# Performance work log

Hardware: AMD Instinct MI355X
Metric: run time of the kernel (lower is better)

Reference implementation:

```python
import jax, jax.numpy as jnp
import numpy as np

IN_DIM, OUT_DIM, N_BLOCKS, BLK_DIM = 256, 4, 2, 128
S, B = 1024, 128


def _u(key, shape, fan):
    lim = 1.0 / np.sqrt(fan)
    return jax.random.uniform(key, shape, jnp.float32, -lim, lim)


def _gru_params(key, i, h):
    k = jax.random.split(key, 4)
    return (_u(k[0], (3 * h, i), h), _u(k[1], (3 * h, h), h),
            _u(k[2], (3 * h,), h), _u(k[3], (3 * h,), h))


def gru_layer(x, wih, whh, bih, bhh):
    # x: (S, B, I) -> outputs (S, B, H); PyTorch GRU gate math, h0 = 0
    Bt = x.shape[1]
    H = whh.shape[1]
    xg = jnp.einsum('sbi,gi->sbg', x, wih) + bih  # (S, B, 3H) precomputed input gates

    def step(h, xg_t):
        hg = h @ whh.T + bhh
        xr, xz, xn = jnp.split(xg_t, 3, axis=-1)
        hr, hz, hn = jnp.split(hg, 3, axis=-1)
        r = jax.nn.sigmoid(xr + hr)
        z = jax.nn.sigmoid(xz + hz)
        n = jnp.tanh(xn + r * hn)
        h_new = (1.0 - z) * n + z * h
        return h_new, h_new

    h0 = jnp.zeros((Bt, H), x.dtype)
    _, ys = jax.lax.scan(step, h0, xg)
    return ys


def layernorm(x, g, b, eps=1e-5):
    m = jnp.mean(x, axis=-1, keepdims=True)
    v = jnp.mean(jnp.square(x - m), axis=-1, keepdims=True)
    return (x - m) * jax.lax.rsqrt(v + eps) * g + b


def setup_inputs() -> dict:
    key = jax.random.key(0)
    ks = jax.random.split(key, 16)
    d = {'x': jax.random.normal(ks[0], (S, B, IN_DIM), jnp.float32)}
    for nm, (i, h), kk in [('gru0', (IN_DIM, 2 * IN_DIM), ks[1]),
                           ('gru1', (IN_DIM // 2, IN_DIM), ks[2]),
                           ('gru2', (IN_DIM // 4, IN_DIM // 2), ks[3])]:
        wih, whh, bih, bhh = _gru_params(kk, i, h)
        d[nm + '_wih'], d[nm + '_whh'], d[nm + '_bih'], d[nm + '_bhh'] = wih, whh, bih, bhh
    d['d0_w'] = _u(ks[4], (BLK_DIM, 3 * 2 * IN_DIM), 3 * 2 * IN_DIM)
    d['d0_b'] = _u(ks[5], (BLK_DIM,), 3 * 2 * IN_DIM)
    for bi in range(N_BLOCKS):
        kb = jax.random.split(ks[6 + bi], 2)
        d[f'blk{bi}_ln_g'] = jnp.ones((BLK_DIM,), jnp.float32)
        d[f'blk{bi}_ln_b'] = jnp.zeros((BLK_DIM,), jnp.float32)
        wih, whh, bih, bhh = _gru_params(kb[0], BLK_DIM, BLK_DIM)
        d[f'blk{bi}_wih'], d[f'blk{bi}_whh'] = wih, whh
        d[f'blk{bi}_bih'], d[f'blk{bi}_bhh'] = bih, bhh
    d['df_w'] = _u(ks[10], (OUT_DIM, BLK_DIM), BLK_DIM)
    d['df_b'] = _u(ks[11], (OUT_DIM,), BLK_DIM)
    return d


def reference(x,
              gru0_wih, gru0_whh, gru0_bih, gru0_bhh,
              gru1_wih, gru1_whh, gru1_bih, gru1_bhh,
              gru2_wih, gru2_whh, gru2_bih, gru2_bhh,
              d0_w, d0_b,
              blk0_ln_g, blk0_ln_b, blk0_wih, blk0_whh, blk0_bih, blk0_bhh,
              blk1_ln_g, blk1_ln_b, blk1_wih, blk1_whh, blk1_bih, blk1_bhh,
              df_w, df_b):
    # branch 0: full-resolution features
    x0 = gru_layer(x, gru0_wih, gru0_whh, gru0_bih, gru0_bhh)            # (S,B,512)
    # branch 1: nearest-downsample features x0.5, GRU, nearest-upsample x2
    x1 = gru_layer(x[..., ::2], gru1_wih, gru1_whh, gru1_bih, gru1_bhh)  # (S,B,256)
    x1 = jnp.repeat(x1, 2, axis=-1)                                       # (S,B,512)
    # branch 2: nearest-downsample features x0.25, GRU, nearest-upsample x4
    x2 = gru_layer(x[..., ::4], gru2_wih, gru2_whh, gru2_bih, gru2_bhh)  # (S,B,128)
    x2 = jnp.repeat(x2, 4, axis=-1)                                       # (S,B,512)
    h = jnp.concatenate((x0, x1, x2), axis=-1)                            # (S,B,1536)
    h = jax.nn.relu(h @ d0_w.T + d0_b)                                    # (S,B,128)
    for (lg, lb, wih, whh, bih, bhh) in (
            (blk0_ln_g, blk0_ln_b, blk0_wih, blk0_whh, blk0_bih, blk0_bhh),
            (blk1_ln_g, blk1_ln_b, blk1_wih, blk1_whh, blk1_bih, blk1_bhh)):
        h = h + gru_layer(layernorm(h, lg, lb), wih, whh, bih, bhh)       # LN->GRU->residual
    return h @ df_w.T + df_b                                              # (S,B,4)
```

## Files before the change

kernel.cpp:

```cpp
#include <hip/hip_runtime.h>

typedef unsigned int u32;
typedef unsigned short u16;
typedef __attribute__((ext_vector_type(8))) short short8;
typedef __attribute__((ext_vector_type(4))) float f4;

#define MFMA16 __builtin_amdgcn_mfma_f32_16x16x32_bf16
#define ALOAD(p)    __hip_atomic_load((p), __ATOMIC_RELAXED, __HIP_MEMORY_SCOPE_AGENT)
#define ASTORE(p,v) __hip_atomic_store((p), (v), __ATOMIC_RELAXED, __HIP_MEMORY_SCOPE_AGENT)

#define OFF_XB    0LL
#define OFF_XD2   67108864LL
#define OFF_XD4   100663296LL
#define OFF_HCAT  117440512LL
#define OFF_LNB   352321536LL
#define OFF_H0R   385875968LL
#define OFF_Y0R   419430400LL
#define OFF_HB0   419561472LL
#define OFF_HB1   419823616LL
#define OFF_FLG   419954688LL
#define OFF_D0WF  420020224LL

__device__ __forceinline__ u16 f2bf(float f) {
  u32 u = __float_as_uint(f);
  return (u16)((u + 0x7fffu + ((u >> 16) & 1u)) >> 16);
}
__device__ __forceinline__ float bf2f(u32 b) { return __uint_as_float(b << 16); }
__device__ __forceinline__ float sigm(float x) { return __builtin_amdgcn_rcpf(1.f + __expf(-x)); }
__device__ __forceinline__ float tanh_(float x) { return 1.f - 2.f * __builtin_amdgcn_rcpf(1.f + __expf(2.f * x)); }

__device__ __forceinline__ short8 cvt8(const float* p) {
  short8 r;
#pragma unroll
  for (int j = 0; j < 8; ++j) r[j] = (short)f2bf(p[j]);
  return r;
}

template<int KH, int KX, int BT, int CSPAN, int WAVES, int GROUP_WGS, int PUB>
__device__ __forceinline__ void gru_scan(
    const float* __restrict__ wih, const float* __restrict__ whh,
    const float* __restrict__ bih, const float* __restrict__ bhh,
    const u16* __restrict__ xsrc,
    u16* __restrict__ outp, const int outPitch, const int outColBase,
    const int group, const int slab,
    u32* __restrict__ hbA, u32* __restrict__ hbB, u32* __restrict__ flags,
    char* sm)
{
  constexpr int H = KH;
  constexpr int KT = (KH + KX) / 32;
  constexpr int KH32 = KH / 32;
  constexpr int PITCH = (KH + KX) * 2 + 32;
  constexpr int CT_N = CSPAN / 16;
  constexpr int NTILES = (BT / 16) * CT_N;
  constexpr int MAXP = (NTILES + WAVES - 1) / WAVES;
  constexpr int NT = WAVES * 64;
  constexpr int NX = (BT * KX / 2) / NT;
  constexpr int NH = (BT * KH / 2) / NT;
  constexpr bool GH = (GROUP_WGS > 0);

  const int tid = threadIdx.x;
  const int l = tid & 63;
  const int wv = __builtin_amdgcn_readfirstlane(tid >> 6);
  const int lr = l & 15;
  const int lh = l >> 4;
  const long srow0 = group * BT;

  short8 Br[MAXP][KT], Bz[MAXP][KT], Bn[MAXP][KT];
  float bb0[MAXP], bb1[MAXP], bb2[MAXP], bb3[MAXP];
  float hk[MAXP][4];
#pragma unroll
  for (int p = 0; p < MAXP; ++p) {
    const int tp = wv + WAVES * p;
    const int tpc = (tp < NTILES) ? tp : 0;
    const int ct = tpc % CT_N;
    const int gcol = slab * CSPAN + ct * 16 + lr;
#pragma unroll
    for (int t = 0; t < KT; ++t) {
      const int k = t * 32 + lh * 8;
      if (t < KH32) {
        Br[p][t] = cvt8(whh + (long)(0 * H + gcol) * KH + k);
        Bz[p][t] = cvt8(whh + (long)(1 * H + gcol) * KH + k);
        Bn[p][t] = cvt8(whh + (long)(2 * H + gcol) * KH + k);
      } else {
        const int kx = k - KH;
        Br[p][t] = cvt8(wih + (long)(0 * H + gcol) * KX + kx);
        Bz[p][t] = cvt8(wih + (long)(1 * H + gcol) * KX + kx);
        Bn[p][t] = cvt8(wih + (long)(2 * H + gcol) * KX + kx);
      }
    }
    bb0[p] = bih[0 * H + gcol] + bhh[0 * H + gcol];
    bb1[p] = bih[1 * H + gcol] + bhh[1 * H + gcol];
    bb2[p] = bih[2 * H + gcol];
    bb3[p] = bhh[2 * H + gcol];
    hk[p][0] = hk[p][1] = hk[p][2] = hk[p][3] = 0.f;
  }

  if constexpr (!GH) {
#pragma unroll
    for (int i = 0; i < (BT * KH / 2 + NT - 1) / NT; ++i) {
      const int idx = tid + NT * i;
      if (idx < BT * KH / 2) {
        const int r = idx / (KH / 2), d = idx % (KH / 2);
        *(u32*)(sm + r * PITCH + ((d * 4) ^ ((r & 7) << 4))) = 0u;
      }
    }
  }

  u32 xr[NX];
#pragma unroll
  for (int i = 0; i < NX; ++i) {
    const int idx = tid + NT * i;
    const int r = idx / (KX / 2), d = idx % (KX / 2);
    xr[i] = *(const u32*)(xsrc + (srow0 + r) * KX + d * 2);
  }

  for (int s = 0; s < 1024; ++s) {
    if constexpr (GH) {
      if (wv == 0) {
        const u32 tgt = (u32)s;
        for (;;) {
          const u32 f = (l < GROUP_WGS) ? ALOAD(flags + l * 16) : tgt;
          if (__all(f >= tgt)) break;
        }
      }
      __builtin_amdgcn_s_barrier();
    }
#pragma unroll
    for (int i = 0; i < NX; ++i) {
      const int idx = tid + NT * i;
      const int r = idx / (KX / 2), d = idx % (KX / 2);
      *(u32*)(sm + r * PITCH + ((KH * 2 + d * 4) ^ ((r & 7) << 4))) = xr[i];
    }
    if constexpr (GH) {
      const u32* hb = (s & 1) ? hbB : hbA;
#pragma unroll
      for (int i = 0; i < NH; ++i) {
        const int idx = tid + NT * i;
        const int r = idx / (KH / 2), d = idx % (KH / 2);
        const u32 v = ALOAD(hb + r * (KH / 2) + d);
        *(u32*)(sm + r * PITCH + ((d * 4) ^ ((r & 7) << 4))) = v;
      }
    }
    if constexpr (!(GH || PUB)) {
      if (s + 1 < 1024) {
#pragma unroll
        for (int i = 0; i < NX; ++i) {
          const int idx = tid + NT * i;
          const int r = idx / (KX / 2), d = idx % (KX / 2);
          xr[i] = *(const u32*)(xsrc + ((s + 1) * 128L + srow0 + r) * KX + d * 2);
        }
      }
    }
    __syncthreads();

    u32 hnew[MAXP][4];
#pragma unroll
    for (int p = 0; p < MAXP; ++p) {
      const int tp = wv + WAVES * p;
      if (tp < NTILES) {
        const int mt = tp / CT_N;
        f4 ar = {0.f, 0.f, 0.f, 0.f}; f4 az = ar, anh = ar, anx = ar;
#pragma unroll
        for (int t = 0; t < KT; ++t) {
          const int row = mt * 16 + lr;
          const short8 a = *(const short8*)(sm + row * PITCH +
                              ((t * 64 + lh * 16) ^ ((row & 7) << 4)));
          ar = MFMA16(a, Br[p][t], ar, 0, 0, 0);
          az = MFMA16(a, Bz[p][t], az, 0, 0, 0);
          if (t < KH32) anh = MFMA16(a, Bn[p][t], anh, 0, 0, 0);
          else          anx = MFMA16(a, Bn[p][t], anx, 0, 0, 0);
        }
#pragma unroll
        for (int q = 0; q < 4; ++q) {
          const float rg = sigm(ar[q] + bb0[p]);
          const float zg = sigm(az[q] + bb1[p]);
          const float ng = tanh_(anx[q] + bb2[p] + rg * (anh[q] + bb3[p]));
          const float h = (1.f - zg) * ng + zg * hk[p][q];
          hk[p][q] = h;
          hnew[p][q] = f2bf(h);
        }
      }
    }
    if constexpr (!GH) __syncthreads();

    u32 pkv[MAXP][4];
#pragma unroll
    for (int p = 0; p < MAXP; ++p) {
      const int tp = wv + WAVES * p;
      if (tp < NTILES) {
        const int mt = tp / CT_N, ct = tp % CT_N;
        const int c = ct * 16 + lr;
#pragma unroll
        for (int q = 0; q < 4; ++q) {
          const u32 nb = (u32)__shfl_xor((int)hnew[p][q], 1);
          pkv[p][q] = (hnew[p][q] & 0xffffu) | (nb << 16);
          if ((l & 1) == 0) {
            const int b = mt * 16 + lh * 4 + q;
            if constexpr (GH) {
              u32* hbn = ((s + 1) & 1) ? hbB : hbA;
              ASTORE(hbn + b * (KH / 2) + (slab * CSPAN + c) / 2, pkv[p][q]);
            } else {
              *(u32*)(sm + b * PITCH + ((c * 2) ^ ((b & 7) << 4))) = pkv[p][q];
            }
          }
        }
      }
    }
    __builtin_amdgcn_sched_barrier(0);
#pragma unroll
    for (int p = 0; p < MAXP; ++p) {
      const int tp = wv + WAVES * p;
      if (tp < NTILES) {
        const int mt = tp / CT_N, ct = tp % CT_N;
        const int c = ct * 16 + lr;
#pragma unroll
        for (int q = 0; q < 4; ++q) {
          if ((l & 1) == 0) {
            const int b = mt * 16 + lh * 4 + q;
            u32* oa = (u32*)(outp + (s * 128L + srow0 + b) * outPitch + outColBase + c);
            if constexpr (GH || PUB) ASTORE(oa, pkv[p][q]); else *oa = pkv[p][q];
          }
        }
      }
    }
    if constexpr (GH) {
      __builtin_amdgcn_sched_barrier(0);
      if (s + 1 < 1024) {
#pragma unroll
        for (int i = 0; i < NX; ++i) {
          const int idx = tid + NT * i;
          const int r = idx / (KX / 2), d = idx % (KX / 2);
          xr[i] = ALOAD((const u32*)(xsrc + ((s + 1) * 128L + srow0 + r) * KX + d * 2));
        }
        __builtin_amdgcn_sched_barrier(0);
        asm volatile("s_waitcnt vmcnt(%0)" :: "i"(MAXP * 4 + NX) : "memory");
      } else {
        asm volatile("s_waitcnt vmcnt(0)" ::: "memory");
      }
      __builtin_amdgcn_s_barrier();
      if (tid == 0) ASTORE(flags + slab * 16, (u32)(s + 1));
    } else if constexpr (PUB) {
      __builtin_amdgcn_sched_barrier(0);
      if (s + 1 < 1024) {
#pragma unroll
        for (int i = 0; i < NX; ++i) {
          const int idx = tid + NT * i;
          const int r = idx / (KX / 2), d = idx % (KX / 2);
          xr[i] = ALOAD((const u32*)(xsrc + ((s + 1) * 128L + srow0 + r) * KX + d * 2));
        }
        __builtin_amdgcn_sched_barrier(0);
        asm volatile("s_waitcnt vmcnt(%0)" :: "i"(NX) : "memory");
      } else {
        asm volatile("s_waitcnt vmcnt(0)" ::: "memory");
      }
      __builtin_amdgcn_s_barrier();
      if (tid == 0) ASTORE(flags, (u32)(s + 1));
    }
  }
}

__device__ __forceinline__ void gru0_scan(
    const float* __restrict__ wih, const float* __restrict__ whh,
    const float* __restrict__ bih, const float* __restrict__ bhh,
    const u16* __restrict__ x, u16* __restrict__ outp,
    const int group, const int slab,
    u32* __restrict__ hbA, u32* __restrict__ hbB, u32* __restrict__ flags,
    char* sm)
{
  constexpr int PITCH = 1568;
  const int tid = threadIdx.x;
  const int l = tid & 63;
  const int wv = __builtin_amdgcn_readfirstlane(tid >> 6);
  const int lr = l & 15, lh = l >> 4;
  const int ct = wv & 3, gg = wv >> 2;
  const long srow0 = group * 16;
  const int gcol = slab * 64 + ct * 16 + lr;
  f4* red = (f4*)(sm + 25088);

  short8 W0[24], W1[16];
#pragma unroll
  for (int t = 0; t < 24; ++t) {
    const int k = t * 32 + lh * 8;
    if (t < 16) W0[t] = cvt8(whh + (long)(gg * 512 + gcol) * 512 + k);
    else        W0[t] = cvt8(wih + (long)(gg * 512 + gcol) * 256 + (k - 512));
  }
  if (gg == 0) {
#pragma unroll
    for (int t = 0; t < 16; ++t)
      W1[t] = cvt8(whh + (long)(2 * 512 + gcol) * 512 + t * 32 + lh * 8);
  } else {
#pragma unroll
    for (int t = 0; t < 8; ++t)
      W1[t] = cvt8(wih + (long)(2 * 512 + gcol) * 256 + t * 32 + lh * 8);
  }
  const float bb0 = bih[0 * 512 + gcol] + bhh[0 * 512 + gcol];
  const float bb1 = bih[1 * 512 + gcol] + bhh[1 * 512 + gcol];
  const float bb2 = bih[2 * 512 + gcol];
  const float bb3 = bhh[2 * 512 + gcol];
  float hk[4] = {0.f, 0.f, 0.f, 0.f};

  u32 xr[4];
#pragma unroll
  for (int i = 0; i < 4; ++i) {
    const int idx = tid + 512 * i;
    const int r = idx >> 7, d = idx & 127;
    xr[i] = *(const u32*)(x + (srow0 + r) * 256 + d * 2);
  }

  for (int s = 0; s < 1024; ++s) {
    if (wv == 0) {
      const u32 tgt = (u32)s;
      for (;;) {
        const u32 f = (l < 8) ? ALOAD(flags + l * 16) : tgt;
        if (__all(f >= tgt)) break;
      }
    }
    __builtin_amdgcn_s_barrier();
#pragma unroll
    for (int i = 0; i < 4; ++i) {
      const int idx = tid + 512 * i;
      const int r = idx >> 7, d = idx & 127;
      *(u32*)(sm + r * PITCH + ((1024 + d * 4) ^ ((r & 7) << 4))) = xr[i];
    }
    {
      const u32* hb = (s & 1) ? hbB : hbA;
#pragma unroll
      for (int i = 0; i < 8; ++i) {
        const int idx = tid + 512 * i;
        const int r = idx >> 8, d = idx & 255;
        const u32 v = ALOAD(hb + r * 256 + d);
        *(u32*)(sm + r * PITCH + ((d * 4) ^ ((r & 7) << 4))) = v;
      }
    }
    __syncthreads();

    f4 a0 = {0.f, 0.f, 0.f, 0.f}, a1 = a0;
    if (gg == 0) {
#pragma unroll
      for (int t = 0; t < 24; ++t) {
        const short8 a = *(const short8*)(sm + lr * PITCH +
                            ((t * 64 + lh * 16) ^ ((lr & 7) << 4)));
        a0 = MFMA16(a, W0[t], a0, 0, 0, 0);
        if (t < 16) a1 = MFMA16(a, W1[t], a1, 0, 0, 0);
      }
    } else {
#pragma unroll
      for (int t = 0; t < 24; ++t) {
        const short8 a = *(const short8*)(sm + lr * PITCH +
                            ((t * 64 + lh * 16) ^ ((lr & 7) << 4)));
        a0 = MFMA16(a, W0[t], a0, 0, 0, 0);
        if (t >= 16) a1 = MFMA16(a, W1[t - 16], a1, 0, 0, 0);
      }
      red[(ct * 2 + 0) * 64 + l] = a0;
      red[(ct * 2 + 1) * 64 + l] = a1;
    }
    __syncthreads();
    u32 pkv[4];
    if (gg == 0) {
      const f4 paz  = red[(ct * 2 + 0) * 64 + l];
      const f4 panx = red[(ct * 2 + 1) * 64 + l];
      u32 hnew[4];
#pragma unroll
      for (int q = 0; q < 4; ++q) {
        const float rg = sigm(a0[q] + bb0);
        const float zg = sigm(paz[q] + bb1);
        const float ng = tanh_(panx[q] + bb2 + rg * (a1[q] + bb3));
        const float h = (1.f - zg) * ng + zg * hk[q];
        hk[q] = h;
        hnew[q] = f2bf(h);
      }
      u32* hbn = ((s + 1) & 1) ? hbB : hbA;
#pragma unroll
      for (int q = 0; q < 4; ++q) {
        const u32 nb = (u32)__shfl_xor((int)hnew[q], 1);
        pkv[q] = (hnew[q] & 0xffffu) | (nb << 16);
        if ((l & 1) == 0) {
          const int b = lh * 4 + q;
          const int c = ct * 16 + lr;
          ASTORE(hbn + b * 256 + (slab * 64 + c) / 2, pkv[q]);
        }
      }
      __builtin_amdgcn_sched_barrier(0);
#pragma unroll
      for (int q = 0; q < 4; ++q) {
        if ((l & 1) == 0) {
          const int b = lh * 4 + q;
          const int c = ct * 16 + lr;
          ASTORE((u32*)(outp + (s * 128L + srow0 + b) * 896 + slab * 64 + c), pkv[q]);
        }
      }
    }
    __builtin_amdgcn_sched_barrier(0);
    if (s + 1 < 1024) {
#pragma unroll
      for (int i = 0; i < 4; ++i) {
        const int idx = tid + 512 * i;
        const int r = idx >> 7, d = idx & 127;
        xr[i] = ALOAD((const u32*)(x + ((s + 1) * 128L + srow0 + r) * 256 + d * 2));
      }
      __builtin_amdgcn_sched_barrier(0);
      asm volatile("s_waitcnt vmcnt(8)" ::: "memory");
    } else {
      asm volatile("s_waitcnt vmcnt(0)" ::: "memory");
    }
    __builtin_amdgcn_s_barrier();
    if (tid == 0) ASTORE(flags + slab * 16, (u32)(s + 1));
  }
}

struct MegaArgs {
  const float *w0ih, *w0hh, *b0ih, *b0hh;
  const float *w1ih, *w1hh, *b1ih, *b1hh;
  const float *w2ih, *w2hh, *b2ih, *b2hh;
  const u16 *xb, *xd2, *xd4;
  u16 *hcat, *lnb;
  u32 *h0r, *y0r, *hbuf0, *hbuf1, *flg;
  const u16 *d0wf; const float *d0b;
  const float *ln0g, *ln0b;
  const float *c0wih, *c0whh, *c0bih, *c0bhh;
  const float *ln1g, *ln1b;
  const float *c1wih, *c1whh, *c1bih, *c1bhh;
  const float *dfw, *dfb;
  float* out;
};

__device__ __forceinline__ void d0ln_scan(const MegaArgs& a, const int g,
                                          const int p, char* sm)
{
  const int tid = threadIdx.x;
  const int l = tid & 63;
  const int wv = __builtin_amdgcn_readfirstlane(tid >> 6);
  const int lr = l & 15, lh = l >> 4;
  const int dcol = wv * 16 + lr;
  u16* sA = (u16*)sm;
  float* part = (float*)(sm + 1536);
  float* rowstat = (float*)(sm + 3584);

  short8 Dw[28];
#pragma unroll
  for (int t = 0; t < 28; ++t)
    Dw[t] = *(const short8*)(a.d0wf + (long)dcol * 896 + t * 32 + lh * 8);
  const float dbias = a.d0b[dcol];
  const float lg = a.ln0g[dcol], lb = a.ln0b[dcol];

  const u32* hcat32 = (const u32*)a.hcat;
  u32* lnb32 = (u32*)a.lnb;
  const u32* pollp;
  if (l < 8)        pollp = a.flg + g * 128 + l * 16;
  else if (l < 16)  pollp = a.flg + 1024 + (g >> 1) * 128 + (l - 8) * 16;
  else if (l == 16) pollp = a.flg + 2048 + g * 16;
  else              pollp = a.flg + 12800 + g * 16;
  const int stg = (tid < 256);
  const int sr = tid >> 4, sc = tid & 15;

  for (int s = p; s < 1024; s += 8) {
    if (wv == 0) {
      const u32 t01 = (u32)((s + 2 < 1024) ? s + 2 : 1024);
      const u32 t2  = (u32)(s + 1);
      for (;;) {
        int ok = 1;
        if (l < 16)       ok = (ALOAD(pollp) >= t01);
        else if (l == 16) ok = (ALOAD(pollp) >= t2);
        else if (l == 17) ok = (ALOAD(pollp) + 512 >= t2);
        if (__all(ok)) break;
        __builtin_amdgcn_s_sleep(32);
      }
    }
    __syncthreads();
    const long rowbase = (long)s * 128 + g * 16;
    f4 acc = {0.f, 0.f, 0.f, 0.f};
    u32 vst = 0;
    if (stg) vst = ALOAD(hcat32 + (rowbase + sr) * 448 + sc);
    for (int kt = 0; kt < 28; ++kt) {
      u32 vnext = 0;
      if (kt + 1 < 28 && stg)
        vnext = ALOAD(hcat32 + (rowbase + sr) * 448 + (kt + 1) * 16 + sc);
      __syncthreads();
      if (stg) *(u32*)((char*)sA + sr * 80 + sc * 4) = vst;
      __syncthreads();
      const short8 af = *(const short8*)((char*)sA + lr * 80 + lh * 16);
      acc = MFMA16(af, Dw[kt], acc, 0, 0, 0);
      vst = vnext;
    }
    float v[4];
#pragma unroll
    for (int q = 0; q < 4; ++q) { const float xv = acc[q] + dbias; v[q] = xv > 0.f ? xv : 0.f; }
#pragma unroll
    for (int q = 0; q < 4; ++q) {
      float s1 = v[q], s2 = v[q] * v[q];
#pragma unroll
      for (int o = 1; o < 16; o <<= 1) { s1 += __shfl_xor(s1, o); s2 += __shfl_xor(s2, o); }
      if (lr == 0) {
        const int row = lh * 4 + q;
        part[(row * 8 + wv) * 2] = s1;
        part[(row * 8 + wv) * 2 + 1] = s2;
      }
    }
    __syncthreads();
    if (tid < 16) {
      float S1 = 0.f, S2 = 0.f;
#pragma unroll
      for (int w = 0; w < 8; ++w) { S1 += part[(tid * 8 + w) * 2]; S2 += part[(tid * 8 + w) * 2 + 1]; }
      const float m = S1 * 0.0078125f;
      const float rs = rsqrtf(S2 * 0.0078125f - m * m + 1e-5f);
      rowstat[tid * 2] = m; rowstat[tid * 2 + 1] = rs;
    }
    __syncthreads();
#pragma unroll
    for (int q = 0; q < 4; ++q) {
      const int row = lh * 4 + q;
      const float m = rowstat[row * 2], rs = rowstat[row * 2 + 1];
      const u16 lnq = f2bf((v[q] - m) * rs * lg + lb);
      const u32 nb = (u32)__shfl_xor((int)(u32)lnq, 1);
      if ((l & 1) == 0)
        ASTORE(lnb32 + (rowbase + row) * 64 + (dcol >> 1), ((u32)lnq & 0xffffu) | (nb << 16));
      ASTORE(a.h0r + ((long)(s & 511) * 128 + g * 16 + row) * 128 + dcol,
             __float_as_uint(v[q]));
    }
    asm volatile("s_waitcnt vmcnt(0)" ::: "memory");
    __syncthreads();
    if (tid == 0) ASTORE(a.flg + 4096 + g * 1024 + s, 1u);
  }
}

__device__ __forceinline__ void b0_scan(const MegaArgs& a, const int g, char* sm)
{
  const int tid = threadIdx.x, l = tid & 63;
  const int wv = __builtin_amdgcn_readfirstlane(tid >> 6);
  const int lr = l & 15, lh = l >> 4;
  const int gcol = wv * 16 + lr;
  char* T = sm;
  short8 Br[8], Bz[8], Bn[8];
#pragma unroll
  for (int t = 0; t < 8; ++t) {
    const int k = t * 32 + lh * 8;
    if (t < 4) {
      Br[t] = cvt8(a.c0whh + (long)(0 * 128 + gcol) * 128 + k);
      Bz[t] = cvt8(a.c0whh + (long)(1 * 128 + gcol) * 128 + k);
      Bn[t] = cvt8(a.c0whh + (long)(2 * 128 + gcol) * 128 + k);
    } else {
      const int kx = k - 128;
      Br[t] = cvt8(a.c0wih + (long)(0 * 128 + gcol) * 128 + kx);
      Bz[t] = cvt8(a.c0wih + (long)(1 * 128 + gcol) * 128 + kx);
      Bn[t] = cvt8(a.c0wih + (long)(2 * 128 + gcol) * 128 + kx);
    }
  }
  const float b0v = a.c0bih[gcol] + a.c0bhh[gcol];
  const float b1v = a.c0bih[128 + gcol] + a.c0bhh[128 + gcol];
  const float b2v = a.c0bih[256 + gcol];
  const float b3v = a.c0bhh[256 + gcol];
  float hk[4] = {0.f, 0.f, 0.f, 0.f};
#pragma unroll
  for (int i = 0; i < 2; ++i) {
    const int idx = tid + 512 * i; const int r = idx >> 6, d = idx & 63;
    *(u32*)(T + r * 544 + ((d * 4) ^ ((r & 7) << 4))) = 0u;
  }
  const u32* lnb32 = (const u32*)a.lnb;
  const u32* d0fp = a.flg + 4096 + g * 1024;
  const u32* ackp = a.flg + 12800 + g * 16;
  u32* myf = a.flg + 12544 + g * 16;
  __syncthreads();
  for (int s = 0; s < 1024; ++s) {
    if (wv == 0) {
      for (;;) {
        u32 f = 1u;
        if (l == 0)      f = ALOAD(d0fp + s);
        else if (l == 1) f = (ALOAD(ackp) + 3 >= (u32)s) ? 1u : 0u;
        if (__all(f >= 1u)) break;
        __builtin_amdgcn_s_sleep(4);
      }
    }
    __syncthreads();
#pragma unroll
    for (int i = 0; i < 2; ++i) {
      const int idx = tid + 512 * i; const int r = idx >> 6, d = idx & 63;
      const u32 xv = ALOAD(lnb32 + ((long)s * 128 + g * 16 + r) * 64 + d);
      *(u32*)(T + r * 544 + ((256 + d * 4) ^ ((r & 7) << 4))) = xv;
    }
    __syncthreads();
    f4 ar = {0.f, 0.f, 0.f, 0.f}; f4 az = ar, anh = ar, anx = ar;
#pragma unroll
    for (int t = 0; t < 8; ++t) {
      const short8 aa = *(const short8*)(T + lr * 544 + ((t * 64 + lh * 16) ^ ((lr & 7) << 4)));
      ar = MFMA16(aa, Br[t], ar, 0, 0, 0);
      az = MFMA16(aa, Bz[t], az, 0, 0, 0);
      if (t < 4) anh = MFMA16(aa, Bn[t], anh, 0, 0, 0);
      else       anx = MFMA16(aa, Bn[t], anx, 0, 0, 0);
    }
    u32 hnew[4];
#pragma unroll
    for (int q = 0; q < 4; ++q) {
      const float rg = sigm(ar[q] + b0v);
      const float zg = sigm(az[q] + b1v);
      const float ng = tanh_(anx[q] + b2v + rg * (anh[q] + b3v));
      const float h = (1.f - zg) * ng + zg * hk[q];
      hk[q] = h; hnew[q] = f2bf(h);
    }
    __syncthreads();
#pragma unroll
    for (int q = 0; q < 4; ++q) {
      const u32 nb = (u32)__shfl_xor((int)hnew[q], 1);
      if ((l & 1) == 0) {
        const u32 pk = (hnew[q] & 0xffffu) | (nb << 16);
        const int b = lh * 4 + q, c = wv * 16 + lr;
        *(u32*)(T + b * 544 + ((c * 2) ^ ((b & 7) << 4))) = pk;
        ASTORE(a.y0r + ((s & 3) * 8 + g) * 1024 + b * 64 + (c >> 1), pk);
      }
    }
    asm volatile("s_waitcnt vmcnt(0)" ::: "memory");
    __syncthreads();
    if (tid == 0) ASTORE(myf, (u32)(s + 1));
  }
}

__device__ __forceinline__ void b1_scan(const MegaArgs& a, const int g, char* sm)
{
  const int tid = threadIdx.x, l = tid & 63;
  const int wv = __builtin_amdgcn_readfirstlane(tid >> 6);
  const int lr = l & 15, lh = l >> 4;
  const int gcol = wv * 16 + lr;
  char* T = sm;
  float* SDF = (float*)(sm + 8704);
  float* SDB = (float*)(sm + 10752);
  short8 Br[8], Bz[8], Bn[8];
#pragma unroll
  for (int t = 0; t < 8; ++t) {
    const int k = t * 32 + lh * 8;
    if (t < 4) {
      Br[t] = cvt8(a.c1whh + (long)(0 * 128 + gcol) * 128 + k);
      Bz[t] = cvt8(a.c1whh + (long)(1 * 128 + gcol) * 128 + k);
      Bn[t] = cvt8(a.c1whh + (long)(2 * 128 + gcol) * 128 + k);
    } else {
      const int kx = k - 128;
      Br[t] = cvt8(a.c1wih + (long)(0 * 128 + gcol) * 128 + kx);
      Bz[t] = cvt8(a.c1wih + (long)(1 * 128 + gcol) * 128 + kx);
      Bn[t] = cvt8(a.c1wih + (long)(2 * 128 + gcol) * 128 + kx);
    }
  }
  const float b0v = a.c1bih[gcol] + a.c1bhh[gcol];
  const float b1v = a.c1bih[128 + gcol] + a.c1bhh[128 + gcol];
  const float b2v = a.c1bih[256 + gcol];
  const float b3v = a.c1bhh[256 + gcol];
  float hk[4] = {0.f, 0.f, 0.f, 0.f};
#pragma unroll
  for (int i = 0; i < 2; ++i) {
    const int idx = tid + 512 * i; const int r = idx >> 6, d = idx & 63;
    *(u32*)(T + r * 544 + ((d * 4) ^ ((r & 7) << 4))) = 0u;
  }
  SDF[tid] = a.dfw[tid];
  if (tid < 4) SDB[tid] = a.dfb[tid];
  const int rr = tid >> 5, cq = tid & 31, c4 = cq * 4;
  const float g1a = a.ln1g[c4], g1b = a.ln1g[c4 + 1], g1c = a.ln1g[c4 + 2], g1d = a.ln1g[c4 + 3];
  const float h1a = a.ln1b[c4], h1b = a.ln1b[c4 + 1], h1c = a.ln1b[c4 + 2], h1d = a.ln1b[c4 + 3];
  const u32* y0fp = a.flg + 12544 + g * 16;
  u32* ackp = a.flg + 12800 + g * 16;
  __syncthreads();
  for (int s = 0; s < 1024; ++s) {
    if (wv == 0) {
      const u32 tgt = (u32)(s + 1);
      for (;;) {
        const u32 f = (l == 0) ? ALOAD(y0fp) : tgt;
        if (__all(f >= tgt)) break;
        __builtin_amdgcn_s_sleep(4);
      }
    }
    __syncthreads();
    const u32 ya = ALOAD(a.y0r + ((s & 3) * 8 + g) * 1024 + rr * 64 + cq * 2);
    const u32 yb = ALOAD(a.y0r + ((s & 3) * 8 + g) * 1024 + rr * 64 + cq * 2 + 1);
    const long hbase = ((long)(s & 511) * 128 + g * 16 + rr) * 128 + c4;
    const float p0 = __uint_as_float(ALOAD(a.h0r + hbase));
    const float p1 = __uint_as_float(ALOAD(a.h0r + hbase + 1));
    const float p2 = __uint_as_float(ALOAD(a.h0r + hbase + 2));
    const float p3 = __uint_as_float(ALOAD(a.h0r + hbase + 3));
    const float u0 = p0 + bf2f(ya & 0xffffu);
    const float u1 = p1 + bf2f(ya >> 16);
    const float u2 = p2 + bf2f(yb & 0xffffu);
    const float u3 = p3 + bf2f(yb >> 16);
    float s1 = u0 + u1 + u2 + u3;
    float s2 = u0 * u0 + u1 * u1 + u2 * u2 + u3 * u3;
#pragma unroll
    for (int o = 1; o < 32; o <<= 1) { s1 += __shfl_xor(s1, o); s2 += __shfl_xor(s2, o); }
    const float m = s1 * 0.0078125f;
    const float rs = rsqrtf(s2 * 0.0078125f - m * m + 1e-5f);
    const u32 q0 = (u32)f2bf((u0 - m) * rs * g1a + h1a) |
                   ((u32)f2bf((u1 - m) * rs * g1b + h1b) << 16);
    const u32 q1 = (u32)f2bf((u2 - m) * rs * g1c + h1c) |
                   ((u32)f2bf((u3 - m) * rs * g1d + h1d) << 16);
    char* xa = T + rr * 544 + ((256 + cq * 8) ^ ((rr & 7) << 4));
    *(u32*)xa = q0;
    *(u32*)(xa + 4) = q1;
    __syncthreads();
    if (tid == 0) ASTORE(ackp, (u32)(s + 1));
    f4 ar = {0.f, 0.f, 0.f, 0.f}; f4 az = ar, anh = ar, anx = ar;
#pragma unroll
    for (int t = 0; t < 8; ++t) {
      const short8 aa = *(const short8*)(T + lr * 544 + ((t * 64 + lh * 16) ^ ((lr & 7) << 4)));
      ar = MFMA16(aa, Br[t], ar, 0, 0, 0);
      az = MFMA16(aa, Bz[t], az, 0, 0, 0);
      if (t < 4) anh = MFMA16(aa, Bn[t], anh, 0, 0, 0);
      else       anx = MFMA16(aa, Bn[t], anx, 0, 0, 0);
    }
    u32 hnew[4];
#pragma unroll
    for (int q = 0; q < 4; ++q) {
      const float rg = sigm(ar[q] + b0v);
      const float zg = sigm(az[q] + b1v);
      const float ng = tanh_(anx[q] + b2v + rg * (anh[q] + b3v));
      const float h = (1.f - zg) * ng + zg * hk[q];
      hk[q] = h; hnew[q] = f2bf(h);
    }
    __syncthreads();
#pragma unroll
    for (int q = 0; q < 4; ++q) {
      const u32 nb = (u32)__shfl_xor((int)hnew[q], 1);
      if ((l & 1) == 0) {
        const u32 pk = (hnew[q] & 0xffffu) | (nb << 16);
        const int b = lh * 4 + q, c = wv * 16 + lr;
        *(u32*)(T + b * 544 + ((c * 2) ^ ((b & 7) << 4))) = pk;
      }
    }
    __syncthreads();
    const int yo = (c4 * 2) ^ ((rr & 7) << 4);
    const u32 za = *(const u32*)(T + rr * 544 + yo);
    const u32 zb = *(const u32*)(T + rr * 544 + yo + 4);
    const float w0 = u0 + bf2f(za & 0xffffu);
    const float w1 = u1 + bf2f(za >> 16);
    const float w2 = u2 + bf2f(zb & 0xffffu);
    const float w3 = u3 + bf2f(zb >> 16);
    float pp0 = w0 * SDF[c4]       + w1 * SDF[c4 + 1]       + w2 * SDF[c4 + 2]       + w3 * SDF[c4 + 3];
    float pp1 = w0 * SDF[128 + c4] + w1 * SDF[128 + c4 + 1] + w2 * SDF[128 + c4 + 2] + w3 * SDF[128 + c4 + 3];
    float pp2 = w0 * SDF[256 + c4] + w1 * SDF[256 + c4 + 1] + w2 * SDF[256 + c4 + 2] + w3 * SDF[256 + c4 + 3];
    float pp3 = w0 * SDF[384 + c4] + w1 * SDF[384 + c4 + 1] + w2 * SDF[384 + c4 + 2] + w3 * SDF[384 + c4 + 3];
#pragma unroll
    for (int o = 1; o < 32; o <<= 1) {
      pp0 += __shfl_xor(pp0, o); pp1 += __shfl_xor(pp1, o);
      pp2 += __shfl_xor(pp2, o); pp3 += __shfl_xor(pp3, o);
    }
    if (cq == 0) {
      f4 ov = {pp0 + SDB[0], pp1 + SDB[1], pp2 + SDB[2], pp3 + SDB[3]};
      *(f4*)(a.out + ((long)s * 128 + g * 16 + rr) * 4) = ov;
    }
  }
}

__global__ void __launch_bounds__(512, 2) mega(MegaArgs a) {
  __shared__ __align__(16) char sm[33280];
  const int bid = blockIdx.x;
  if (bid < 64) {
    const int group = bid & 7, slab = bid >> 3;
    gru0_scan(a.w0ih, a.w0hh, a.b0ih, a.b0hh, a.xb, a.hcat, group, slab,
              a.hbuf0 + group * 4096, a.hbuf0 + 32768 + group * 4096,
              a.flg + group * 128, sm);
  } else if (bid < 96) {
    const int id = bid - 64, G = id & 3, slab = id >> 2;
    gru_scan<256, 128, 32, 32, 8, 8, 0>(a.w1ih, a.w1hh, a.b1ih, a.b1hh, a.xd2,
        a.hcat, 896, 512 + slab * 32, G, slab,
        a.hbuf1 + G * 4096, a.hbuf1 + 16384 + G * 4096,
        a.flg + 1024 + G * 128, sm);
  } else if (bid < 104) {
    const int g = bid - 96;
    gru_scan<128, 64, 16, 128, 8, 0, 1>(a.w2ih, a.w2hh, a.b2ih, a.b2hh, a.xd4,
        a.hcat, 896, 768, g, 0, nullptr, nullptr,
        a.flg + 2048 + g * 16, sm);
  } else if (bid < 168) {
    const int id = bid - 104;
    d0ln_scan(a, id & 7, id >> 3, sm);
  } else if (bid < 176) {
    b0_scan(a, bid - 168, sm);
  } else {
    b1_scan(a, bid - 176, sm);
  }
}

__global__ void __launch_bounds__(256) prep(const float* __restrict__ x,
    u16* __restrict__ xb, u16* __restrict__ xd2, u16* __restrict__ xd4,
    const float* __restrict__ d0w, u16* __restrict__ d0wf) {
  const int b = blockIdx.x;
  if (b < 16384) {
    const long t = b * 256L + threadIdx.x;
    const f4 aa = ((const f4*)x)[t * 2];
    const f4 cc = ((const f4*)x)[t * 2 + 1];
    const u16 u0 = f2bf(aa[0]), u1 = f2bf(aa[1]), u2 = f2bf(aa[2]), u3 = f2bf(aa[3]);
    const u16 u4 = f2bf(cc[0]), u5 = f2bf(cc[1]), u6 = f2bf(cc[2]), u7 = f2bf(cc[3]);
    short8 s8; s8[0]=(short)u0; s8[1]=(short)u1; s8[2]=(short)u2; s8[3]=(short)u3;
    s8[4]=(short)u4; s8[5]=(short)u5; s8[6]=(short)u6; s8[7]=(short)u7;
    *(short8*)(xb + t * 8) = s8;
    const long row = t >> 5; const int ch = (int)(t & 31);
    *(u32*)(xd2 + row * 128 + ch * 4)     = (u32)u0 | ((u32)u2 << 16);
    *(u32*)(xd2 + row * 128 + ch * 4 + 2) = (u32)u4 | ((u32)u6 << 16);
    *(u32*)(xd4 + row * 64 + ch * 2)      = (u32)u0 | ((u32)u4 << 16);
  } else {
    const int idx = (b - 16384) * 256 + threadIdx.x;
    const int o = idx / 896, c = idx % 896;
    float v;
    if (c < 512) v = d0w[o * 1536 + c];
    else if (c < 768) { const int j = c - 512; v = d0w[o * 1536 + 512 + 2 * j] + d0w[o * 1536 + 513 + 2 * j]; }
    else { const int j = c - 768; const float* p = d0w + o * 1536 + 1024 + 4 * j; v = p[0] + p[1] + p[2] + p[3]; }
    d0wf[idx] = f2bf(v);
  }
}

extern "C" void kernel_launch(void* const* d_in, const int* in_sizes, int n_in,
                              void* d_out, int out_size, void* d_ws, size_t ws_size,
                              hipStream_t stream) {
  char* ws = (char*)d_ws;
  const float* x     = (const float*)d_in[0];
  const float* g0wih = (const float*)d_in[1];
  const float* g0whh = (const float*)d_in[2];
  const float* g0bih = (const float*)d_in[3];
  const float* g0bhh = (const float*)d_in[4];
  const float* g1wih = (const float*)d_in[5];
  const float* g1whh = (const float*)d_in[6];
  const float* g1bih = (const float*)d_in[7];
  const float* g1bhh = (const float*)d_in[8];
  const float* g2wih = (const float*)d_in[9];
  const float* g2whh = (const float*)d_in[10];
  const float* g2bih = (const float*)d_in[11];
  const float* g2bhh = (const float*)d_in[12];
  const float* d0w   = (const float*)d_in[13];
  const float* d0b   = (const float*)d_in[14];
  const float* ln0g  = (const float*)d_in[15];
  const float* ln0b  = (const float*)d_in[16];
  const float* b0wih = (const float*)d_in[17];
  const float* b0whh = (const float*)d_in[18];
  const float* b0bih = (const float*)d_in[19];
  const float* b0bhh = (const float*)d_in[20];
  const float* ln1g  = (const float*)d_in[21];
  const float* ln1b  = (const float*)d_in[22];
  const float* b1wih = (const float*)d_in[23];
  const float* b1whh = (const float*)d_in[24];
  const float* b1bih = (const float*)d_in[25];
  const float* b1bhh = (const float*)d_in[26];
  const float* dfw   = (const float*)d_in[27];
  const float* dfb   = (const float*)d_in[28];

  MegaArgs a;
  a.w0ih = g0wih; a.w0hh = g0whh; a.b0ih = g0bih; a.b0hh = g0bhh;
  a.w1ih = g1wih; a.w1hh = g1whh; a.b1ih = g1bih; a.b1hh = g1bhh;
  a.w2ih = g2wih; a.w2hh = g2whh; a.b2ih = g2bih; a.b2hh = g2bhh;
  a.xb  = (u16*)(ws + OFF_XB);
  a.xd2 = (u16*)(ws + OFF_XD2);
  a.xd4 = (u16*)(ws + OFF_XD4);
  a.hcat = (u16*)(ws + OFF_HCAT);
  a.lnb  = (u16*)(ws + OFF_LNB);
  a.h0r  = (u32*)(ws + OFF_H0R);
  a.y0r  = (u32*)(ws + OFF_Y0R);
  a.hbuf0 = (u32*)(ws + OFF_HB0);
  a.hbuf1 = (u32*)(ws + OFF_HB1);
  a.flg   = (u32*)(ws + OFF_FLG);
  a.d0wf  = (u16*)(ws + OFF_D0WF);
  a.d0b = d0b; a.ln0g = ln0g; a.ln0b = ln0b;
  a.c0wih = b0wih; a.c0whh = b0whh; a.c0bih = b0bih; a.c0bhh = b0bhh;
  a.ln1g = ln1g; a.ln1b = ln1b;
  a.c1wih = b1wih; a.c1whh = b1whh; a.c1bih = b1bih; a.c1bhh = b1bhh;
  a.dfw = dfw; a.dfb = dfb;
  a.out = (float*)d_out;

  hipMemsetAsync(ws + OFF_HB0, 0, (size_t)(OFF_D0WF - OFF_HB0), stream);

  prep<<<16832, 256, 0, stream>>>(x, (u16*)(ws + OFF_XB), (u16*)(ws + OFF_XD2),
                                  (u16*)(ws + OFF_XD4), d0w, (u16*)(ws + OFF_D0WF));

  mega<<<184, 512, 0, stream>>>(a);
}
```

Baseline: 4.568 ms.

## Overlap x-input MFMAs with the cross-block hidden-state wait in GRU0

Moves the input-projection MFMAs (k-tiles 16..23, which read the x slice) ahead of the flag spin-wait so they run while other slabs finish producing h. Each wave now waits only on the one producer flag it needs and copies its own 32-column slice of h into LDS, instead of wave 0 polling all flags. The next step's x is prefetched early and written to LDS at the end of the step. The __syncthreads calls are replaced with explicit waitcnt plus s_barrier. This shortens the serial dependency chain per timestep, but the finer-grained sync is more fragile and the changed vmcnt accounting must stay correct.

```diff
diff --git a/kernel.cpp b/kernel.cpp
--- a/kernel.cpp
+++ b/kernel.cpp
@@ -306,55 +306,80 @@
     const int r = idx >> 7, d = idx & 127;
     xr[i] = *(const u32*)(x + (srow0 + r) * 256 + d * 2);
   }
+#pragma unroll
+  for (int i = 0; i < 4; ++i) {
+    const int idx = tid + 512 * i;
+    const int r = idx >> 7, d = idx & 127;
+    *(u32*)(sm + r * PITCH + ((1024 + d * 4) ^ ((r & 7) << 4))) = xr[i];
+  }
+  __syncthreads();
 
   for (int s = 0; s < 1024; ++s) {
-    if (wv == 0) {
-      const u32 tgt = (u32)s;
-      for (;;) {
-        const u32 f = (l < 8) ? ALOAD(flags + l * 16) : tgt;
-        if (__all(f >= tgt)) break;
-      }
-    }
-    __builtin_amdgcn_s_barrier();
-#pragma unroll
-    for (int i = 0; i < 4; ++i) {
-      const int idx = tid + 512 * i;
-      const int r = idx >> 7, d = idx & 127;
-      *(u32*)(sm + r * PITCH + ((1024 + d * 4) ^ ((r & 7) << 4))) = xr[i];
-    }
-    {
-      const u32* hb = (s & 1) ? hbB : hbA;
-#pragma unroll
-      for (int i = 0; i < 8; ++i) {
-        const int idx = tid + 512 * i;
-        const int r = idx >> 8, d = idx & 255;
-        const u32 v = ALOAD(hb + r * 256 + d);
-        *(u32*)(sm + r * PITCH + ((d * 4) ^ ((r & 7) << 4))) = v;
-      }
-    }
-    __syncthreads();
-
     f4 a0 = {0.f, 0.f, 0.f, 0.f}, a1 = a0;
     if (gg == 0) {
 #pragma unroll
-      for (int t = 0; t < 24; ++t) {
+      for (int t = 16; t < 24; ++t) {
         const short8 a = *(const short8*)(sm + lr * PITCH +
                             ((t * 64 + lh * 16) ^ ((lr & 7) << 4)));
         a0 = MFMA16(a, W0[t], a0, 0, 0, 0);
-        if (t < 16) a1 = MFMA16(a, W1[t], a1, 0, 0, 0);
       }
     } else {
 #pragma unroll
-      for (int t = 0; t < 24; ++t) {
+      for (int t = 16; t < 24; ++t) {
         const short8 a = *(const short8*)(sm + lr * PITCH +
                             ((t * 64 + lh * 16) ^ ((lr & 7) << 4)));
         a0 = MFMA16(a, W0[t], a0, 0, 0, 0);
-        if (t >= 16) a1 = MFMA16(a, W1[t - 16], a1, 0, 0, 0);
+        a1 = MFMA16(a, W1[t - 16], a1, 0, 0, 0);
+      }
+    }
+    if (s + 1 < 1024) {
+#pragma unroll
+      for (int i = 0; i < 4; ++i) {
+        const int idx = tid + 512 * i;
+        const int r = idx >> 7, d = idx & 127;
+        xr[i] = ALOAD((const u32*)(x + ((s + 1) * 128L + srow0 + r) * 256 + d * 2));
+      }
+    }
+    for (;;) {
+      const u32 f = ALOAD(flags + wv * 16);
+      if (__builtin_amdgcn_readfirstlane(f) >= (u32)s) break;
+    }
+    {
+      const u32* hb = (s & 1) ? hbB : hbA;
+#pragma unroll
+      for (int i = 0; i < 8; ++i) {
+        const int idx = l + 64 * i;
+        const int r = idx >> 5, d = idx & 31;
+        const u32 v = ALOAD(hb + r * 256 + wv * 32 + d);
+        *(u32*)(sm + r * PITCH + ((wv * 128 + d * 4) ^ ((r & 7) << 4))) = v;
+      }
+    }
+    asm volatile("s_waitcnt lgkmcnt(0)" ::: "memory");
+    __builtin_amdgcn_sched_barrier(0);
+    __builtin_amdgcn_s_barrier();
+    __builtin_amdgcn_sched_barrier(0);
+    if (gg == 0) {
+#pragma unroll
+      for (int t = 0; t < 16; ++t) {
+        const short8 a = *(const short8*)(sm + lr * PITCH +
+                            ((t * 64 + lh * 16) ^ ((lr & 7) << 4)));
+        a0 = MFMA16(a, W0[t], a0, 0, 0, 0);
+        a1 = MFMA16(a, W1[t], a1, 0, 0, 0);
+      }
+    } else {
+#pragma unroll
+      for (int t = 0; t < 16; ++t) {
+        const short8 a = *(const short8*)(sm + lr * PITCH +
+                            ((t * 64 + lh * 16) ^ ((lr & 7) << 4)));
+        a0 = MFMA16(a, W0[t], a0, 0, 0, 0);
       }
       red[(ct * 2 + 0) * 64 + l] = a0;
       red[(ct * 2 + 1) * 64 + l] = a1;
     }
-    __syncthreads();
+    asm volatile("s_waitcnt lgkmcnt(0)" ::: "memory");
+    __builtin_amdgcn_sched_barrier(0);
+    __builtin_amdgcn_s_barrier();
+    __builtin_amdgcn_sched_barrier(0);
     u32 pkv[4];
     if (gg == 0) {
       const f4 paz  = red[(ct * 2 + 0) * 64 + l];
@@ -396,14 +421,15 @@
       for (int i = 0; i < 4; ++i) {
         const int idx = tid + 512 * i;
         const int r = idx >> 7, d = idx & 127;
-        xr[i] = ALOAD((const u32*)(x + ((s + 1) * 128L + srow0 + r) * 256 + d * 2));
+        *(u32*)(sm + r * PITCH + ((1024 + d * 4) ^ ((r & 7) << 4))) = xr[i];
       }
       __builtin_amdgcn_sched_barrier(0);
-      asm volatile("s_waitcnt vmcnt(8)" ::: "memory");
+      asm volatile("s_waitcnt vmcnt(4) lgkmcnt(0)" ::: "memory");
     } else {
-      asm volatile("s_waitcnt vmcnt(0)" ::: "memory");
+      asm volatile("s_waitcnt vmcnt(0) lgkmcnt(0)" ::: "memory");
     }
     __builtin_amdgcn_s_barrier();
+    __builtin_amdgcn_sched_barrier(0);
     if (tid == 0) ASTORE(flags + slab * 16, (u32)(s + 1));
   }
 }
```

Result: no change. 4.540 ms (median of 2 runs) (-0.6%).
